# Kernel optimization log

Hardware: AMD Instinct MI355X
Metric: run time of the kernel (lower is better)

Reference implementation:

```python
import jax, jax.numpy as jnp
import numpy as np

B, Q, C, N_PER, GS = 8, 2048, 256, 64, 8
H1, H2 = 256, 64
EPS = 1e-5


def make_grid():
    a = jnp.linspace(-0.1, 0.1, GS)
    gx, gy = jnp.meshgrid(a, a, indexing='ij')  # torch.meshgrid default 'ij'
    return jnp.stack([gx.reshape(-1), gy.reshape(-1)], axis=1)  # (n, 2)


def setup_inputs() -> dict:
    key = jax.random.key(0)
    ks = jax.random.split(key, 10)
    s = lambda k, shp, fan: jax.random.normal(k, shp, jnp.float32) / np.sqrt(fan)
    return {
        'tokens': jax.random.normal(ks[0], (B, Q, C), jnp.float32),
        'grid': make_grid(),
        'Wc': s(ks[1], (C, 3), C), 'bc': jnp.zeros((3,), jnp.float32),
        'W1': s(ks[2], (C + 2, H1), C + 2), 'b1': jnp.zeros((H1,), jnp.float32),
        'gamma1': jnp.ones((H1,), jnp.float32), 'beta1': jnp.zeros((H1,), jnp.float32),
        'W2': s(ks[3], (H1, H2), H1), 'b2': jnp.zeros((H2,), jnp.float32),
        'gamma2': jnp.ones((H2,), jnp.float32), 'beta2': jnp.zeros((H2,), jnp.float32),
        'W3': s(ks[4], (H2, 3), H2), 'b3': jnp.zeros((3,), jnp.float32),
    }


def batchnorm(x, gamma, beta):
    # BatchNorm1d in training mode: stats over batch (B*Q) and length (n) dims,
    # per channel (last axis here).
    mean = jnp.mean(x, axis=(0, 1, 2), keepdims=True)
    var = jnp.var(x, axis=(0, 1, 2), keepdims=True)
    return gamma * (x - mean) * jax.lax.rsqrt(var + EPS) + beta


def reference(tokens, grid, Wc, bc, W1, b1, gamma1, beta1, W2, b2, gamma2, beta2, W3, b3):
    coarse = tokens @ Wc + bc  # (B, Q, 3)
    # conv1 (1x1) on concat([tokens_expanded, grid]) == split matmul + broadcast add;
    # avoids materializing the (B,Q,n,C+2) concat explicitly.
    tok_part = tokens @ W1[:C]                 # (B, Q, H1)
    grid_part = grid @ W1[C:]                  # (n, H1)
    h = tok_part[:, :, None, :] + grid_part[None, None, :, :] + b1  # (B, Q, n, H1)
    h = jax.nn.relu(batchnorm(h, gamma1, beta1))
    h = jnp.einsum('bqnc,cd->bqnd', h, W2) + b2  # (B, Q, n, H2)
    h = jax.nn.relu(batchnorm(h, gamma2, beta2))
    disp = jnp.einsum('bqnc,cd->bqnd', h, W3) + b3  # (B, Q, n, 3)
    fine = (coarse[:, :, None, :] + disp).reshape(B, Q * N_PER, 3)
    return coarse, fine
```

## Files before the change

kernel.cpp:

```cpp
#include <hip/hip_runtime.h>
#include <hip/hip_bf16.h>

#define ROWS 16384
#define C_   256
#define H1_  256
#define H2_  64
#define EPSN 1e-5f

typedef __bf16 bf16x8 __attribute__((ext_vector_type(8)));
typedef __bf16 bf16x4 __attribute__((ext_vector_type(4)));
typedef __bf16 bf16x2 __attribute__((ext_vector_type(2)));
typedef float  f32x4  __attribute__((ext_vector_type(4)));
typedef float  f32x2  __attribute__((ext_vector_type(2)));

__device__ __forceinline__ bf16x2 cvt2(float a, float b) {
#if __has_builtin(__builtin_amdgcn_cvt_pk_bf16_f32)
    return __builtin_bit_cast(bf16x2, __builtin_amdgcn_cvt_pk_bf16_f32(a, b));
#else
    bf16x2 r; r[0] = (__bf16)a; r[1] = (__bf16)b; return r;
#endif
}

__global__ __launch_bounds__(256) void k0_pack(const float* __restrict__ W1,
                                               const float* __restrict__ W2,
                                               const float* __restrict__ W3,
                                               __bf16* __restrict__ W1p,
                                               __bf16* __restrict__ W2p,
                                               __bf16* __restrict__ W3p,
                                               float* __restrict__ zero_base) {
    int idx = blockIdx.x * 256 + threadIdx.x;
    if (idx < 65536) {
        int j = idx & 7, l = (idx >> 3) & 63, rest = idx >> 9;
        int ks = rest & 7, CT = rest >> 3;
        int k = ks * 32 + ((l >> 4) << 3) + j;
        int c = CT * 16 + (l & 15);
        W1p[idx] = (__bf16)W1[k * H1_ + c];
    } else {
        int i2 = idx - 65536;
        int j = i2 & 7, l = (i2 >> 3) & 63, rest = i2 >> 9;
        int ks = rest & 7, CK = rest >> 3;
        int k = ks * 32 + ((l >> 4) << 3) + j;
        int c2 = CK * 16 + (l & 15);
        W2p[i2] = (__bf16)W2[k * H2_ + c2];
    }
    if (idx < 1024) {
        int j = idx & 7, l = (idx >> 3) & 63, ks = idx >> 9;
        int k = ks * 32 + ((l >> 4) << 3) + j;
        int c = l & 15;
        W3p[idx] = (c < 3) ? (__bf16)W3[k * 3 + c] : (__bf16)0.f;
    }
    if (idx < 24576) zero_base[idx] = 0.0f;
}

__device__ __forceinline__ void prep_ctx(const float* __restrict__ grid,
                                         const float* __restrict__ W1,
                                         const float* __restrict__ a1p, int c0,
                                         f32x2* wgx2, f32x2* wgy2, float* A_) {
#pragma unroll
    for (int j = 0; j < 8; ++j) A_[j] = grid[2 * j + 1];
    f32x4 a0 = *(const f32x4*)(a1p + c0), a1h = *(const f32x4*)(a1p + c0 + 4);
    f32x4 x0 = *(const f32x4*)(W1 + C_ * H1_ + c0), x1 = *(const f32x4*)(W1 + C_ * H1_ + c0 + 4);
    f32x4 y0 = *(const f32x4*)(W1 + (C_ + 1) * H1_ + c0), yh = *(const f32x4*)(W1 + (C_ + 1) * H1_ + c0 + 4);
    float av[8] = {a0[0], a0[1], a0[2], a0[3], a1h[0], a1h[1], a1h[2], a1h[3]};
    float wx[8] = {x0[0], x0[1], x0[2], x0[3], x1[0], x1[1], x1[2], x1[3]};
    float wy[8] = {y0[0], y0[1], y0[2], y0[3], yh[0], yh[1], yh[2], yh[3]};
#pragma unroll
    for (int e = 0; e < 4; ++e) {
        wgx2[e][0] = av[2 * e] * wx[2 * e];     wgx2[e][1] = av[2 * e + 1] * wx[2 * e + 1];
        wgy2[e][0] = av[2 * e] * wy[2 * e];     wgy2[e][1] = av[2 * e + 1] * wy[2 * e + 1];
    }
}

__device__ __forceinline__ void stage16(__bf16* __restrict__ y1, int w, int c0, int nh,
                                        const float* __restrict__ a1p,
                                        const float* __restrict__ d1p,
                                        const f32x2* wgx2, const f32x2* wgy2,
                                        const float* A_,
                                        const float* __restrict__ tokrow) {
    f32x4 t0 = *(const f32x4*)(tokrow + c0);
    f32x4 t1 = *(const f32x4*)(tokrow + c0 + 4);
    f32x4 a0 = *(const f32x4*)(a1p + c0), a1h = *(const f32x4*)(a1p + c0 + 4);
    f32x4 d0 = *(const f32x4*)(d1p + c0), d1h = *(const f32x4*)(d1p + c0 + 4);
    f32x2 base2[4];
    base2[0][0] = fmaf(a0[0], t0[0], d0[0]);  base2[0][1] = fmaf(a0[1], t0[1], d0[1]);
    base2[1][0] = fmaf(a0[2], t0[2], d0[2]);  base2[1][1] = fmaf(a0[3], t0[3], d0[3]);
    base2[2][0] = fmaf(a1h[0], t1[0], d1h[0]); base2[2][1] = fmaf(a1h[1], t1[1], d1h[1]);
    base2[3][0] = fmaf(a1h[2], t1[2], d1h[2]); base2[3][1] = fmaf(a1h[3], t1[3], d1h[3]);
#pragma unroll
    for (int ih = 0; ih < 2; ++ih) {
        float axs = A_[2 * w + ih];
        f32x2 ax2 = {axs, axs};
        f32x2 tc2[4];
#pragma unroll
        for (int e = 0; e < 4; ++e) tc2[e] = __builtin_elementwise_fma(wgx2[e], ax2, base2[e]);
#pragma unroll
        for (int kk = 0; kk < 4; ++kk) {
            int iy = nh + 2 * kk;
            float ays = A_[iy];
            f32x2 ay2 = {ays, ays};
            f32x2 z = {0.f, 0.f};
            int n = w * 16 + ih * 8 + iy;
            bf16x8 out;
            bf16x2* o2 = (bf16x2*)&out;
#pragma unroll
            for (int e = 0; e < 4; ++e) {
                f32x2 v = __builtin_elementwise_max(
                    __builtin_elementwise_fma(wgy2[e], ay2, tc2[e]), z);
                o2[e] = cvt2(v[0], v[1]);
            }
            *(bf16x8*)(&y1[n * 264 + c0]) = out;
        }
    }
}

__global__ __launch_bounds__(256) void k1a(const float* __restrict__ tokens,
                                           const __bf16* __restrict__ W1p,
                                           const float* __restrict__ Wc,
                                           const float* __restrict__ bc,
                                           float* __restrict__ tokpart,
                                           float* __restrict__ coarse,
                                           float* __restrict__ p1s,
                                           float* __restrict__ p1q) {
    __shared__ __align__(16) __bf16 Al[16 * 264];
    int t = threadIdx.x, w = t >> 6, l = t & 63;
    int quad = l >> 4, col = l & 15;
    int rowbase = (blockIdx.x >> 1) * 16;
    int colhalf = blockIdx.x & 1;
    int slot = blockIdx.x & 31;

    bf16x8 bfr[16];
#pragma unroll
    for (int ctl = 0; ctl < 2; ++ctl)
#pragma unroll
        for (int ks = 0; ks < 8; ++ks) {
            int CT = colhalf * 8 + w * 2 + ctl;
            bfr[ctl * 8 + ks] = *(const bf16x8*)(W1p + (((CT * 8 + ks) * 64 + l) * 8));
        }
    {
        int r = t >> 4, cb = (t & 15) * 16;
        const float* src = tokens + (size_t)(rowbase + r) * C_ + cb;
        f32x4 t0 = *(const f32x4*)(src);
        f32x4 t1 = *(const f32x4*)(src + 4);
        f32x4 t2 = *(const f32x4*)(src + 8);
        f32x4 t3 = *(const f32x4*)(src + 12);
        bf16x8 v0, v1;
        bf16x2* p0 = (bf16x2*)&v0; bf16x2* p1 = (bf16x2*)&v1;
        p0[0] = cvt2(t0[0], t0[1]); p0[1] = cvt2(t0[2], t0[3]);
        p0[2] = cvt2(t1[0], t1[1]); p0[3] = cvt2(t1[2], t1[3]);
        p1[0] = cvt2(t2[0], t2[1]); p1[1] = cvt2(t2[2], t2[3]);
        p1[2] = cvt2(t3[0], t3[1]); p1[3] = cvt2(t3[2], t3[3]);
        *(bf16x8*)(&Al[r * 264 + cb]) = v0;
        *(bf16x8*)(&Al[r * 264 + cb + 8]) = v1;
    }
    __syncthreads();

    bf16x8 af[8];
#pragma unroll
    for (int ks = 0; ks < 8; ++ks)
        af[ks] = *(const bf16x8*)(&Al[col * 264 + ks * 32 + quad * 8]);

#pragma unroll
    for (int ctl = 0; ctl < 2; ++ctl) {
        f32x4 acc = {0.f, 0.f, 0.f, 0.f};
#pragma unroll
        for (int ks = 0; ks < 8; ++ks)
            acc = __builtin_amdgcn_mfma_f32_16x16x32_bf16(af[ks], bfr[ctl * 8 + ks], acc, 0, 0, 0);
        int c = colhalf * 128 + w * 32 + ctl * 16 + col;
        float s = 0.f, q = 0.f;
#pragma unroll
        for (int rr = 0; rr < 4; ++rr) {
            float v = acc[rr];
            tokpart[(size_t)(rowbase + quad * 4 + rr) * C_ + c] = v;
            s += v; q += v * v;
        }
        s += __shfl_xor(s, 16, 64); s += __shfl_xor(s, 32, 64);
        q += __shfl_xor(q, 16, 64); q += __shfl_xor(q, 32, 64);
        if (l < 16) {
            int cc = colhalf * 128 + w * 32 + ctl * 16 + l;
            atomicAdd(p1s + slot * C_ + cc, s);
            atomicAdd(p1q + slot * C_ + cc, q);
        }
    }
    if (colhalf == 0) {
        const f32x4* wcp = (const f32x4*)(Wc + l * 12);
        f32x4 wa = wcp[0], wb = wcp[1], wv = wcp[2];
        float wcl[12] = {wa[0], wa[1], wa[2], wa[3], wb[0], wb[1], wb[2], wb[3],
                         wv[0], wv[1], wv[2], wv[3]};
#pragma unroll
        for (int rr = 0; rr < 4; ++rr) {
            int r = w * 4 + rr;
            bf16x4 tv4 = *(const bf16x4*)(&Al[r * 264 + l * 4]);
            float p[3] = {0.f, 0.f, 0.f};
#pragma unroll
            for (int i = 0; i < 4; ++i) {
                float tvf = (float)tv4[i];
#pragma unroll
                for (int j = 0; j < 3; ++j) p[j] = fmaf(tvf, wcl[i * 3 + j], p[j]);
            }
#pragma unroll
            for (int off = 1; off < 64; off <<= 1)
#pragma unroll
                for (int j = 0; j < 3; ++j) p[j] += __shfl_xor(p[j], off, 64);
            if (l == 0) {
#pragma unroll
                for (int j = 0; j < 3; ++j)
                    coarse[(size_t)(rowbase + r) * 3 + j] = p[j] + bc[j];
            }
        }
    }
}

__global__ void k1b(const float* __restrict__ grid, const float* __restrict__ W1,
                    const float* __restrict__ gamma1, const float* __restrict__ beta1,
                    const float* __restrict__ p1s, const float* __restrict__ p1q,
                    float* __restrict__ a1o, float* __restrict__ d1o) {
    int t = threadIdx.x;
    float S = 0.f, Qq = 0.f;
    for (int s = 0; s < 32; ++s) { S += p1s[s * C_ + t]; Qq += p1q[s * C_ + t]; }
    float mean_t = S / (float)ROWS;
    float var_t = Qq / (float)ROWS - mean_t * mean_t;
    float wx = W1[C_ * H1_ + t];
    float wy = W1[(C_ + 1) * H1_ + t];
    float mg = 0.f, qg = 0.f;
    for (int n = 0; n < 64; ++n) {
        float gv = grid[2 * n] * wx + grid[2 * n + 1] * wy;
        mg += gv; qg += gv * gv;
    }
    mg *= (1.f / 64.f);
    float var_g = qg * (1.f / 64.f) - mg * mg;
    float a1 = gamma1[t] * rsqrtf(var_t + var_g + EPSN);
    a1o[t] = a1;
    d1o[t] = beta1[t] - a1 * (mean_t + mg);
}

template <bool SPILL>
__global__ __launch_bounds__(256) void k2(const float* __restrict__ tokpart,
                                          const float* __restrict__ grid,
                                          const float* __restrict__ W1,
                                          const __bf16* __restrict__ W2p,
                                          const float* __restrict__ a1,
                                          const float* __restrict__ d1,
                                          float* __restrict__ p2s,
                                          float* __restrict__ p2q,
                                          __bf16* __restrict__ h2s) {
    __shared__ __align__(16) __bf16 y1[64 * 264];
    __shared__ __align__(16) __bf16 y2l[SPILL ? 64 * 72 : 8];
    int t = threadIdx.x, w = t >> 6, l = t & 63;
    int quad = l >> 4, col = l & 15;
    int wn = w >> 1, wc = w & 1;
    int c0 = (l & 31) * 8, nh = l >> 5;

    bf16x8 bfr[16];
#pragma unroll
    for (int ck = 0; ck < 2; ++ck)
#pragma unroll
        for (int ks = 0; ks < 8; ++ks)
            bfr[ck * 8 + ks] = *(const bf16x8*)(W2p + ((((wc * 2 + ck) * 8 + ks) * 64 + l) * 8));

    f32x2 wgx2[4], wgy2[4]; float A_[8];
    prep_ctx(grid, W1, a1, c0, wgx2, wgy2, A_);

    float s[2][4] = {}, q[2][4] = {};

#pragma unroll 1
    for (int r8 = 0; r8 < 8; ++r8) {
        int row = blockIdx.x * 8 + r8;
        stage16(y1, w, c0, nh, a1, d1, wgx2, wgy2, A_, tokpart + (size_t)row * C_);
        __syncthreads();
#pragma unroll
        for (int rt = 0; rt < 2; ++rt) {
            bf16x8 af[8];
#pragma unroll
            for (int ks = 0; ks < 8; ++ks)
                af[ks] = *(const bf16x8*)(&y1[(wn * 32 + rt * 16 + col) * 264 + ks * 32 + quad * 8]);
#pragma unroll
            for (int ck = 0; ck < 2; ++ck) {
                f32x4 acc = {0.f, 0.f, 0.f, 0.f};
#pragma unroll
                for (int ks = 0; ks < 8; ++ks)
                    acc = __builtin_amdgcn_mfma_f32_16x16x32_bf16(bfr[ck * 8 + ks], af[ks], acc, 0, 0, 0);
#pragma unroll
                for (int rr = 0; rr < 4; ++rr) {
                    s[ck][rr] += acc[rr];
                    q[ck][rr] += acc[rr] * acc[rr];
                }
                if constexpr (SPILL) {
                    bf16x4 v; bf16x2* v2 = (bf16x2*)&v;
                    v2[0] = cvt2(acc[0], acc[1]);
                    v2[1] = cvt2(acc[2], acc[3]);
                    *(bf16x4*)(&y2l[(wn * 32 + rt * 16 + col) * 72 + wc * 32 + ck * 16 + quad * 4]) = v;
                }
            }
        }
        __syncthreads();
        if constexpr (SPILL) {
            int n = t >> 2, cb = (t & 3) * 16;
            bf16x8 u0 = *(const bf16x8*)(&y2l[n * 72 + cb]);
            bf16x8 u1 = *(const bf16x8*)(&y2l[n * 72 + cb + 8]);
            __bf16* dst = h2s + (size_t)row * 4096 + t * 16;
            *(bf16x8*)dst = u0;
            *(bf16x8*)(dst + 8) = u1;
        }
    }
    int slot = blockIdx.x & 63;
#pragma unroll
    for (int ck = 0; ck < 2; ++ck)
#pragma unroll
        for (int rr = 0; rr < 4; ++rr) {
            float sv = s[ck][rr], qv = q[ck][rr];
            sv += __shfl_xor(sv, 1, 64); sv += __shfl_xor(sv, 2, 64);
            sv += __shfl_xor(sv, 4, 64); sv += __shfl_xor(sv, 8, 64);
            qv += __shfl_xor(qv, 1, 64); qv += __shfl_xor(qv, 2, 64);
            qv += __shfl_xor(qv, 4, 64); qv += __shfl_xor(qv, 8, 64);
            if (col == 0) {
                int c2 = wc * 32 + ck * 16 + quad * 4 + rr;
                atomicAdd(p2s + slot * H2_ + c2, sv);
                atomicAdd(p2q + slot * H2_ + c2, qv);
            }
        }
}

__global__ void k2b(const float* __restrict__ p2s, const float* __restrict__ p2q,
                    const float* __restrict__ gamma2, const float* __restrict__ beta2,
                    float* __restrict__ a2o, float* __restrict__ d2o) {
    int t = threadIdx.x;
    float S = 0.f, Qq = 0.f;
    for (int s = 0; s < 64; ++s) { S += p2s[s * H2_ + t]; Qq += p2q[s * H2_ + t]; }
    const float invN = 1.f / ((float)ROWS * 64.f);
    float mean = S * invN;
    float var = Qq * invN - mean * mean;
    float a2 = gamma2[t] * rsqrtf(var + EPSN);
    a2o[t] = a2;
    d2o[t] = beta2[t] - a2 * mean;
}

__global__ __launch_bounds__(256) void k3s(const __bf16* __restrict__ h2s,
                                           const float* __restrict__ a2,
                                           const float* __restrict__ d2p,
                                           const __bf16* __restrict__ W3p,
                                           const float* __restrict__ b3,
                                           const float* __restrict__ coarse,
                                           float* __restrict__ fine) {
    __shared__ __align__(16) __bf16 y2l[8][64 * 72];
    __shared__ __align__(16) float finebuf[8 * 192];
    int t = threadIdx.x, w = t >> 6, l = t & 63;
    int quad = l >> 4, col = l & 15;

    bf16x8 wfr[2];
#pragma unroll
    for (int ks = 0; ks < 2; ++ks)
        wfr[ks] = *(const bf16x8*)(W3p + ((ks * 64 + l) * 8));

    int n = t >> 2, cb = (t & 3) * 16;
    float a2r[16], d2r[16];
#pragma unroll
    for (int i = 0; i < 16; i += 4) {
        f32x4 av = *(const f32x4*)(a2 + cb + i);
        f32x4 dv = *(const f32x4*)(d2p + cb + i);
#pragma unroll
        for (int e = 0; e < 4; ++e) { a2r[i + e] = av[e]; d2r[i + e] = dv[e]; }
    }
#pragma unroll 1
    for (int r8 = 0; r8 < 8; ++r8) {
        size_t row = (size_t)blockIdx.x * 8 + r8;
        const __bf16* src = h2s + row * 4096 + t * 16;
        bf16x8 u0 = *(const bf16x8*)src;
        bf16x8 u1 = *(const bf16x8*)(src + 8);
        bf16x8 o0, o1;
        bf16x2* p0 = (bf16x2*)&o0; bf16x2* p1 = (bf16x2*)&o1;
#pragma unroll
        for (int e = 0; e < 4; ++e) {
            p0[e] = cvt2(fmaxf(fmaf(a2r[2 * e],     (float)u0[2 * e],     d2r[2 * e]), 0.f),
                         fmaxf(fmaf(a2r[2 * e + 1], (float)u0[2 * e + 1], d2r[2 * e + 1]), 0.f));
            p1[e] = cvt2(fmaxf(fmaf(a2r[8 + 2 * e],     (float)u1[2 * e],     d2r[8 + 2 * e]), 0.f),
                         fmaxf(fmaf(a2r[8 + 2 * e + 1], (float)u1[2 * e + 1], d2r[8 + 2 * e + 1]), 0.f));
        }
        *(bf16x8*)(&y2l[r8][n * 72 + cb]) = o0;
        *(bf16x8*)(&y2l[r8][n * 72 + cb + 8]) = o1;
    }
    __syncthreads();
    float b3v = (col < 3) ? b3[col] : 0.f;
#pragma unroll 1
    for (int r8 = 0; r8 < 8; ++r8) {
        int row = blockIdx.x * 8 + r8;
        bf16x8 af2[2];
#pragma unroll
        for (int ks = 0; ks < 2; ++ks)
            af2[ks] = *(const bf16x8*)(&y2l[r8][(w * 16 + col) * 72 + ks * 32 + quad * 8]);
        f32x4 acc = {0.f, 0.f, 0.f, 0.f};
        acc = __builtin_amdgcn_mfma_f32_16x16x32_bf16(af2[0], wfr[0], acc, 0, 0, 0);
        acc = __builtin_amdgcn_mfma_f32_16x16x32_bf16(af2[1], wfr[1], acc, 0, 0, 0);
        if (col < 3) {
            float cj = coarse[row * 3 + col] + b3v;
#pragma unroll
            for (int rr = 0; rr < 4; ++rr)
                finebuf[r8 * 192 + (w * 16 + quad * 4 + rr) * 3 + col] = acc[rr] + cj;
        }
    }
    __syncthreads();
    {
        float* dst = fine + (size_t)blockIdx.x * 1536;
        const f32x4* fb = (const f32x4*)finebuf;
        *(f32x4*)(dst + 4 * t) = fb[t];
        if (t < 128) *(f32x4*)(dst + 1024 + 4 * t) = fb[256 + t];
    }
}

__global__ __launch_bounds__(256) void k3r(const float* __restrict__ tokpart,
                                           const float* __restrict__ grid,
                                           const float* __restrict__ W1,
                                           const __bf16* __restrict__ W2p,
                                           const float* __restrict__ a1,
                                           const float* __restrict__ d1,
                                           const __bf16* __restrict__ W3p,
                                           const float* __restrict__ a2,
                                           const float* __restrict__ d2p,
                                           const float* __restrict__ b3,
                                           const float* __restrict__ coarse,
                                           float* __restrict__ fine) {
    __shared__ __align__(16) __bf16 y1[64 * 264];
    __shared__ __align__(16) __bf16 y2l[64 * 72];
    __shared__ __align__(16) float finebuf[8 * 192];
    int t = threadIdx.x, w = t >> 6, l = t & 63;
    int quad = l >> 4, col = l & 15;
    int wn = w >> 1, wc = w & 1;
    int c0 = (l & 31) * 8, nh = l >> 5;

    bf16x8 bfr[16];
#pragma unroll
    for (int ck = 0; ck < 2; ++ck)
#pragma unroll
        for (int ks = 0; ks < 8; ++ks)
            bfr[ck * 8 + ks] = *(const bf16x8*)(W2p + ((((wc * 2 + ck) * 8 + ks) * 64 + l) * 8));
    bf16x8 wfr[2];
#pragma unroll
    for (int ks = 0; ks < 2; ++ks)
        wfr[ks] = *(const bf16x8*)(W3p + ((ks * 64 + l) * 8));

    f32x2 wgx2[4], wgy2[4]; float A_[8];
    prep_ctx(grid, W1, a1, c0, wgx2, wgy2, A_);

    float a2v[8], d2v[8];
#pragma unroll
    for (int ck = 0; ck < 2; ++ck)
#pragma unroll
        for (int rr = 0; rr < 4; ++rr) {
            int c2 = wc * 32 + ck * 16 + quad * 4 + rr;
            a2v[ck * 4 + rr] = a2[c2];
            d2v[ck * 4 + rr] = d2p[c2];
        }
    float b3v = (col < 3) ? b3[col] : 0.f;

#pragma unroll 1
    for (int r8 = 0; r8 < 8; ++r8) {
        int row = blockIdx.x * 8 + r8;
        stage16(y1, w, c0, nh, a1, d1, wgx2, wgy2, A_, tokpart + (size_t)row * C_);
        __syncthreads();
#pragma unroll
        for (int rt = 0; rt < 2; ++rt) {
            bf16x8 af[8];
#pragma unroll
            for (int ks = 0; ks < 8; ++ks)
                af[ks] = *(const bf16x8*)(&y1[(wn * 32 + rt * 16 + col) * 264 + ks * 32 + quad * 8]);
#pragma unroll
            for (int ck = 0; ck < 2; ++ck) {
                f32x4 acc = {0.f, 0.f, 0.f, 0.f};
#pragma unroll
                for (int ks = 0; ks < 8; ++ks)
                    acc = __builtin_amdgcn_mfma_f32_16x16x32_bf16(bfr[ck * 8 + ks], af[ks], acc, 0, 0, 0);
                bf16x4 v; bf16x2* v2 = (bf16x2*)&v;
                float y0 = fmaxf(fmaf(a2v[ck * 4 + 0], acc[0], d2v[ck * 4 + 0]), 0.f);
                float y1v = fmaxf(fmaf(a2v[ck * 4 + 1], acc[1], d2v[ck * 4 + 1]), 0.f);
                float y2 = fmaxf(fmaf(a2v[ck * 4 + 2], acc[2], d2v[ck * 4 + 2]), 0.f);
                float y3 = fmaxf(fmaf(a2v[ck * 4 + 3], acc[3], d2v[ck * 4 + 3]), 0.f);
                v2[0] = cvt2(y0, y1v); v2[1] = cvt2(y2, y3);
                *(bf16x4*)(&y2l[(wn * 32 + rt * 16 + col) * 72 + wc * 32 + ck * 16 + quad * 4]) = v;
            }
        }
        __syncthreads();
        bf16x8 af2[2];
#pragma unroll
        for (int ks = 0; ks < 2; ++ks)
            af2[ks] = *(const bf16x8*)(&y2l[(w * 16 + col) * 72 + ks * 32 + quad * 8]);
        f32x4 d2acc = {0.f, 0.f, 0.f, 0.f};
        d2acc = __builtin_amdgcn_mfma_f32_16x16x32_bf16(af2[0], wfr[0], d2acc, 0, 0, 0);
        d2acc = __builtin_amdgcn_mfma_f32_16x16x32_bf16(af2[1], wfr[1], d2acc, 0, 0, 0);
        if (col < 3) {
            float cj = coarse[row * 3 + col] + b3v;
#pragma unroll
            for (int rr = 0; rr < 4; ++rr)
                finebuf[r8 * 192 + (w * 16 + quad * 4 + rr) * 3 + col] = d2acc[rr] + cj;
        }
    }
    __syncthreads();
    {
        float* dst = fine + (size_t)blockIdx.x * 1536;
        const f32x4* fb = (const f32x4*)finebuf;
        *(f32x4*)(dst + 4 * t) = fb[t];
        if (t < 128) *(f32x4*)(dst + 1024 + 4 * t) = fb[256 + t];
    }
}

extern "C" void kernel_launch(void* const* d_in, const int* in_sizes, int n_in,
                              void* d_out, int out_size, void* d_ws, size_t ws_size,
                              hipStream_t stream) {
    (void)in_sizes; (void)n_in; (void)out_size;
    const float* tokens = (const float*)d_in[0];
    const float* grid   = (const float*)d_in[1];
    const float* Wc     = (const float*)d_in[2];
    const float* bc     = (const float*)d_in[3];
    const float* W1     = (const float*)d_in[4];
    const float* gamma1 = (const float*)d_in[6];
    const float* beta1  = (const float*)d_in[7];
    const float* W2     = (const float*)d_in[8];
    const float* gamma2 = (const float*)d_in[10];
    const float* beta2  = (const float*)d_in[11];
    const float* W3     = (const float*)d_in[12];
    const float* b3     = (const float*)d_in[13];

    char* ws = (char*)d_ws;
    __bf16* W1p     = (__bf16*)(ws);
    __bf16* W2p     = (__bf16*)(ws + 131072);
    float*  p1s     = (float*)(ws + 163840);
    float*  p1q     = (float*)(ws + 196608);
    float*  p2s     = (float*)(ws + 229376);
    float*  p2q     = (float*)(ws + 245760);
    float*  a1      = (float*)(ws + 262144);
    float*  d1      = (float*)(ws + 263168);
    float*  a2      = (float*)(ws + 264192);
    float*  d2p     = (float*)(ws + 264448);
    __bf16* W3p     = (__bf16*)(ws + 264704);
    float*  tokpart = (float*)(ws + 266752);
    __bf16* h2s     = (__bf16*)(ws + 17043968);

    const size_t SPILL_NEED = 17043968ull + 134217728ull;
    bool spill = ws_size >= SPILL_NEED;

    float* coarse = (float*)d_out;
    float* fine   = (float*)d_out + (size_t)ROWS * 3;

    k0_pack<<<320, 256, 0, stream>>>(W1, W2, W3, W1p, W2p, W3p, p1s);
    k1a<<<2048, 256, 0, stream>>>(tokens, W1p, Wc, bc, tokpart, coarse, p1s, p1q);
    k1b<<<1, 256, 0, stream>>>(grid, W1, gamma1, beta1, p1s, p1q, a1, d1);
    if (spill) {
        k2<true><<<ROWS / 8, 256, 0, stream>>>(tokpart, grid, W1, W2p, a1, d1, p2s, p2q, h2s);
        k2b<<<1, 64, 0, stream>>>(p2s, p2q, gamma2, beta2, a2, d2p);
        k3s<<<ROWS / 8, 256, 0, stream>>>(h2s, a2, d2p, W3p, b3, coarse, fine);
    } else {
        k2<false><<<ROWS / 8, 256, 0, stream>>>(tokpart, grid, W1, W2p, a1, d1, p2s, p2q, h2s);
        k2b<<<1, 64, 0, stream>>>(p2s, p2q, gamma2, beta2, a2, d2p);
        k3r<<<ROWS / 8, 256, 0, stream>>>(tokpart, grid, W1, W2p, a1, d1, W3p, a2, d2p, b3, coarse, fine);
    }
}
```

Measured before the change: 212.4 us.

## Build layer-1 activations in registers and recompute layer 2 instead of spilling

The BN1 affine is pre-folded into the token projection (kfold), and the grid contribution is precomputed per lane. Each lane then forms its MFMA A-fragment directly in registers, so the y1 shared-memory staging and its barriers go away. The h2 spill path is dropped, and layer 2 is recomputed in k3x. Blocks now cover half of the 64 grid points, which doubles the grid size. This trades the 128MB bf16 spill round trip, plus LDS traffic, for one extra fp32 tokfold buffer and repeated per-lane token loads.

```diff
diff --git a/kernel.cpp b/kernel.cpp
--- a/kernel.cpp
+++ b/kernel.cpp
@@ -52,67 +52,6 @@
     if (idx < 24576) zero_base[idx] = 0.0f;
 }
 
-__device__ __forceinline__ void prep_ctx(const float* __restrict__ grid,
-                                         const float* __restrict__ W1,
-                                         const float* __restrict__ a1p, int c0,
-                                         f32x2* wgx2, f32x2* wgy2, float* A_) {
-#pragma unroll
-    for (int j = 0; j < 8; ++j) A_[j] = grid[2 * j + 1];
-    f32x4 a0 = *(const f32x4*)(a1p + c0), a1h = *(const f32x4*)(a1p + c0 + 4);
-    f32x4 x0 = *(const f32x4*)(W1 + C_ * H1_ + c0), x1 = *(const f32x4*)(W1 + C_ * H1_ + c0 + 4);
-    f32x4 y0 = *(const f32x4*)(W1 + (C_ + 1) * H1_ + c0), yh = *(const f32x4*)(W1 + (C_ + 1) * H1_ + c0 + 4);
-    float av[8] = {a0[0], a0[1], a0[2], a0[3], a1h[0], a1h[1], a1h[2], a1h[3]};
-    float wx[8] = {x0[0], x0[1], x0[2], x0[3], x1[0], x1[1], x1[2], x1[3]};
-    float wy[8] = {y0[0], y0[1], y0[2], y0[3], yh[0], yh[1], yh[2], yh[3]};
-#pragma unroll
-    for (int e = 0; e < 4; ++e) {
-        wgx2[e][0] = av[2 * e] * wx[2 * e];     wgx2[e][1] = av[2 * e + 1] * wx[2 * e + 1];
-        wgy2[e][0] = av[2 * e] * wy[2 * e];     wgy2[e][1] = av[2 * e + 1] * wy[2 * e + 1];
-    }
-}
-
-__device__ __forceinline__ void stage16(__bf16* __restrict__ y1, int w, int c0, int nh,
-                                        const float* __restrict__ a1p,
-                                        const float* __restrict__ d1p,
-                                        const f32x2* wgx2, const f32x2* wgy2,
-                                        const float* A_,
-                                        const float* __restrict__ tokrow) {
-    f32x4 t0 = *(const f32x4*)(tokrow + c0);
-    f32x4 t1 = *(const f32x4*)(tokrow + c0 + 4);
-    f32x4 a0 = *(const f32x4*)(a1p + c0), a1h = *(const f32x4*)(a1p + c0 + 4);
-    f32x4 d0 = *(const f32x4*)(d1p + c0), d1h = *(const f32x4*)(d1p + c0 + 4);
-    f32x2 base2[4];
-    base2[0][0] = fmaf(a0[0], t0[0], d0[0]);  base2[0][1] = fmaf(a0[1], t0[1], d0[1]);
-    base2[1][0] = fmaf(a0[2], t0[2], d0[2]);  base2[1][1] = fmaf(a0[3], t0[3], d0[3]);
-    base2[2][0] = fmaf(a1h[0], t1[0], d1h[0]); base2[2][1] = fmaf(a1h[1], t1[1], d1h[1]);
-    base2[3][0] = fmaf(a1h[2], t1[2], d1h[2]); base2[3][1] = fmaf(a1h[3], t1[3], d1h[3]);
-#pragma unroll
-    for (int ih = 0; ih < 2; ++ih) {
-        float axs = A_[2 * w + ih];
-        f32x2 ax2 = {axs, axs};
-        f32x2 tc2[4];
-#pragma unroll
-        for (int e = 0; e < 4; ++e) tc2[e] = __builtin_elementwise_fma(wgx2[e], ax2, base2[e]);
-#pragma unroll
-        for (int kk = 0; kk < 4; ++kk) {
-            int iy = nh + 2 * kk;
-            float ays = A_[iy];
-            f32x2 ay2 = {ays, ays};
-            f32x2 z = {0.f, 0.f};
-            int n = w * 16 + ih * 8 + iy;
-            bf16x8 out;
-            bf16x2* o2 = (bf16x2*)&out;
-#pragma unroll
-            for (int e = 0; e < 4; ++e) {
-                f32x2 v = __builtin_elementwise_max(
-                    __builtin_elementwise_fma(wgy2[e], ay2, tc2[e]), z);
-                o2[e] = cvt2(v[0], v[1]);
-            }
-            *(bf16x8*)(&y1[n * 264 + c0]) = out;
-        }
-    }
-}
-
 __global__ __launch_bounds__(256) void k1a(const float* __restrict__ tokens,
                                            const __bf16* __restrict__ W1p,
                                            const float* __restrict__ Wc,
@@ -213,7 +152,8 @@
 __global__ void k1b(const float* __restrict__ grid, const float* __restrict__ W1,
                     const float* __restrict__ gamma1, const float* __restrict__ beta1,
                     const float* __restrict__ p1s, const float* __restrict__ p1q,
-                    float* __restrict__ a1o, float* __restrict__ d1o) {
+                    float* __restrict__ a1o, float* __restrict__ d1o,
+                    float* __restrict__ wgxo, float* __restrict__ wgyo) {
     int t = threadIdx.x;
     float S = 0.f, Qq = 0.f;
     for (int s = 0; s < 32; ++s) { S += p1s[s * C_ + t]; Qq += p1q[s * C_ + t]; }
@@ -231,93 +171,101 @@
     float a1 = gamma1[t] * rsqrtf(var_t + var_g + EPSN);
     a1o[t] = a1;
     d1o[t] = beta1[t] - a1 * (mean_t + mg);
-}
-
-template <bool SPILL>
-__global__ __launch_bounds__(256) void k2(const float* __restrict__ tokpart,
-                                          const float* __restrict__ grid,
-                                          const float* __restrict__ W1,
-                                          const __bf16* __restrict__ W2p,
-                                          const float* __restrict__ a1,
-                                          const float* __restrict__ d1,
-                                          float* __restrict__ p2s,
-                                          float* __restrict__ p2q,
-                                          __bf16* __restrict__ h2s) {
-    __shared__ __align__(16) __bf16 y1[64 * 264];
-    __shared__ __align__(16) __bf16 y2l[SPILL ? 64 * 72 : 8];
+    wgxo[t] = a1 * wx;
+    wgyo[t] = a1 * wy;
+}
+
+__global__ __launch_bounds__(256) void kfold(const float* __restrict__ tokpart,
+                                             const float* __restrict__ a1,
+                                             const float* __restrict__ d1,
+                                             float* __restrict__ tokfold) {
+    int idx = blockIdx.x * 256 + threadIdx.x;
+    int c0 = (idx * 4) & 255;
+    f32x4 a = *(const f32x4*)(a1 + c0);
+    f32x4 d = *(const f32x4*)(d1 + c0);
+    f32x4 v = *(const f32x4*)(tokpart + (size_t)idx * 4);
+    *(f32x4*)(tokfold + (size_t)idx * 4) = __builtin_elementwise_fma(a, v, d);
+}
+
+__global__ __launch_bounds__(256) void k2x(const float* __restrict__ tokfold,
+                                           const float* __restrict__ grid,
+                                           const __bf16* __restrict__ W2p,
+                                           const float* __restrict__ wgx,
+                                           const float* __restrict__ wgy,
+                                           float* __restrict__ p2s,
+                                           float* __restrict__ p2q) {
     int t = threadIdx.x, w = t >> 6, l = t & 63;
     int quad = l >> 4, col = l & 15;
     int wn = w >> 1, wc = w & 1;
-    int c0 = (l & 31) * 8, nh = l >> 5;
+    int rowgrp = blockIdx.x >> 1, nh = blockIdx.x & 1;
+    int n = nh * 32 + wn * 16 + col;
+    float gx = grid[2 * n], gy = grid[2 * n + 1];
 
     bf16x8 bfr[16];
 #pragma unroll
     for (int ck = 0; ck < 2; ++ck)
 #pragma unroll
-        for (int ks = 0; ks < 8; ++ks)
-            bfr[ck * 8 + ks] = *(const bf16x8*)(W2p + ((((wc * 2 + ck) * 8 + ks) * 64 + l) * 8));
-
-    f32x2 wgx2[4], wgy2[4]; float A_[8];
-    prep_ctx(grid, W1, a1, c0, wgx2, wgy2, A_);
-
-    float s[2][4] = {}, q[2][4] = {};
+        for (int ks = 0; ks < 8; ++ks) {
+            int CK = wc * 2 + ck;
+            bfr[ck * 8 + ks] = *(const bf16x8*)(W2p + (((CK * 8 + ks) * 64 + l) * 8));
+        }
+
+    f32x4 gt[16];
+    f32x4 gx4 = {gx, gx, gx, gx}, gy4 = {gy, gy, gy, gy};
+#pragma unroll
+    for (int ks = 0; ks < 8; ++ks) {
+        int cb = ks * 32 + quad * 8;
+        f32x4 wx0 = *(const f32x4*)(wgx + cb), wx1 = *(const f32x4*)(wgx + cb + 4);
+        f32x4 wy0 = *(const f32x4*)(wgy + cb), wy1 = *(const f32x4*)(wgy + cb + 4);
+        gt[2 * ks]     = __builtin_elementwise_fma(gy4, wy0, gx4 * wx0);
+        gt[2 * ks + 1] = __builtin_elementwise_fma(gy4, wy1, gx4 * wx1);
+    }
+
+    float s[8] = {}, q[8] = {};
+    const f32x4 z4 = {0.f, 0.f, 0.f, 0.f};
 
 #pragma unroll 1
     for (int r8 = 0; r8 < 8; ++r8) {
-        int row = blockIdx.x * 8 + r8;
-        stage16(y1, w, c0, nh, a1, d1, wgx2, wgy2, A_, tokpart + (size_t)row * C_);
-        __syncthreads();
-#pragma unroll
-        for (int rt = 0; rt < 2; ++rt) {
-            bf16x8 af[8];
+        const float* tr = tokfold + (size_t)(rowgrp * 8 + r8) * C_;
+        bf16x8 af[8];
+#pragma unroll
+        for (int ks = 0; ks < 8; ++ks) {
+            int cb = ks * 32 + quad * 8;
+            f32x4 t0 = *(const f32x4*)(tr + cb);
+            f32x4 t1 = *(const f32x4*)(tr + cb + 4);
+            f32x4 v0 = __builtin_elementwise_max(t0 + gt[2 * ks], z4);
+            f32x4 v1 = __builtin_elementwise_max(t1 + gt[2 * ks + 1], z4);
+            bf16x2* o = (bf16x2*)&af[ks];
+            o[0] = cvt2(v0[0], v0[1]); o[1] = cvt2(v0[2], v0[3]);
+            o[2] = cvt2(v1[0], v1[1]); o[3] = cvt2(v1[2], v1[3]);
+        }
+#pragma unroll
+        for (int ck = 0; ck < 2; ++ck) {
+            f32x4 acc = {0.f, 0.f, 0.f, 0.f};
 #pragma unroll
             for (int ks = 0; ks < 8; ++ks)
-                af[ks] = *(const bf16x8*)(&y1[(wn * 32 + rt * 16 + col) * 264 + ks * 32 + quad * 8]);
-#pragma unroll
-            for (int ck = 0; ck < 2; ++ck) {
-                f32x4 acc = {0.f, 0.f, 0.f, 0.f};
-#pragma unroll
-                for (int ks = 0; ks < 8; ++ks)
-                    acc = __builtin_amdgcn_mfma_f32_16x16x32_bf16(bfr[ck * 8 + ks], af[ks], acc, 0, 0, 0);
-#pragma unroll
-                for (int rr = 0; rr < 4; ++rr) {
-                    s[ck][rr] += acc[rr];
-                    q[ck][rr] += acc[rr] * acc[rr];
-                }
-                if constexpr (SPILL) {
-                    bf16x4 v; bf16x2* v2 = (bf16x2*)&v;
-                    v2[0] = cvt2(acc[0], acc[1]);
-                    v2[1] = cvt2(acc[2], acc[3]);
-                    *(bf16x4*)(&y2l[(wn * 32 + rt * 16 + col) * 72 + wc * 32 + ck * 16 + quad * 4]) = v;
-                }
+                acc = __builtin_amdgcn_mfma_f32_16x16x32_bf16(bfr[ck * 8 + ks], af[ks], acc, 0, 0, 0);
+#pragma unroll
+            for (int rr = 0; rr < 4; ++rr) {
+                s[ck * 4 + rr] += acc[rr];
+                q[ck * 4 + rr] = fmaf(acc[rr], acc[rr], q[ck * 4 + rr]);
             }
         }
-        __syncthreads();
-        if constexpr (SPILL) {
-            int n = t >> 2, cb = (t & 3) * 16;
-            bf16x8 u0 = *(const bf16x8*)(&y2l[n * 72 + cb]);
-            bf16x8 u1 = *(const bf16x8*)(&y2l[n * 72 + cb + 8]);
-            __bf16* dst = h2s + (size_t)row * 4096 + t * 16;
-            *(bf16x8*)dst = u0;
-            *(bf16x8*)(dst + 8) = u1;
-        }
     }
     int slot = blockIdx.x & 63;
 #pragma unroll
-    for (int ck = 0; ck < 2; ++ck)
-#pragma unroll
-        for (int rr = 0; rr < 4; ++rr) {
-            float sv = s[ck][rr], qv = q[ck][rr];
-            sv += __shfl_xor(sv, 1, 64); sv += __shfl_xor(sv, 2, 64);
-            sv += __shfl_xor(sv, 4, 64); sv += __shfl_xor(sv, 8, 64);
-            qv += __shfl_xor(qv, 1, 64); qv += __shfl_xor(qv, 2, 64);
-            qv += __shfl_xor(qv, 4, 64); qv += __shfl_xor(qv, 8, 64);
-            if (col == 0) {
-                int c2 = wc * 32 + ck * 16 + quad * 4 + rr;
-                atomicAdd(p2s + slot * H2_ + c2, sv);
-                atomicAdd(p2q + slot * H2_ + c2, qv);
-            }
-        }
+    for (int i = 0; i < 8; ++i) {
+        float sv = s[i], qv = q[i];
+        sv += __shfl_xor(sv, 1, 64); sv += __shfl_xor(sv, 2, 64);
+        sv += __shfl_xor(sv, 4, 64); sv += __shfl_xor(sv, 8, 64);
+        qv += __shfl_xor(qv, 1, 64); qv += __shfl_xor(qv, 2, 64);
+        qv += __shfl_xor(qv, 4, 64); qv += __shfl_xor(qv, 8, 64);
+        if (col == 0) {
+            int c2 = wc * 32 + (i >> 2) * 16 + quad * 4 + (i & 3);
+            atomicAdd(p2s + slot * H2_ + c2, sv);
+            atomicAdd(p2q + slot * H2_ + c2, qv);
+        }
+    }
 }
 
 __global__ void k2b(const float* __restrict__ p2s, const float* __restrict__ p2q,
@@ -334,177 +282,122 @@
     d2o[t] = beta2[t] - a2 * mean;
 }
 
-__global__ __launch_bounds__(256) void k3s(const __bf16* __restrict__ h2s,
+__global__ __launch_bounds__(256) void k3x(const float* __restrict__ tokfold,
+                                           const float* __restrict__ grid,
+                                           const __bf16* __restrict__ W2p,
+                                           const float* __restrict__ wgx,
+                                           const float* __restrict__ wgy,
                                            const float* __restrict__ a2,
                                            const float* __restrict__ d2p,
                                            const __bf16* __restrict__ W3p,
                                            const float* __restrict__ b3,
                                            const float* __restrict__ coarse,
                                            float* __restrict__ fine) {
-    __shared__ __align__(16) __bf16 y2l[8][64 * 72];
-    __shared__ __align__(16) float finebuf[8 * 192];
+    __shared__ __align__(16) __bf16 y2l[8 * 32 * 72];
+    __shared__ __align__(16) float finebuf[8 * 96];
     int t = threadIdx.x, w = t >> 6, l = t & 63;
     int quad = l >> 4, col = l & 15;
-
+    int wn = w >> 1, wc = w & 1;
+    int rowgrp = blockIdx.x >> 1, nh = blockIdx.x & 1;
+    int n = nh * 32 + wn * 16 + col;
+    float gx = grid[2 * n], gy = grid[2 * n + 1];
+
+    bf16x8 bfr[16];
+#pragma unroll
+    for (int ck = 0; ck < 2; ++ck)
+#pragma unroll
+        for (int ks = 0; ks < 8; ++ks) {
+            int CK = wc * 2 + ck;
+            bfr[ck * 8 + ks] = *(const bf16x8*)(W2p + (((CK * 8 + ks) * 64 + l) * 8));
+        }
+    f32x4 gt[16];
+    f32x4 gx4 = {gx, gx, gx, gx}, gy4 = {gy, gy, gy, gy};
+#pragma unroll
+    for (int ks = 0; ks < 8; ++ks) {
+        int cb = ks * 32 + quad * 8;
+        f32x4 wx0 = *(const f32x4*)(wgx + cb), wx1 = *(const f32x4*)(wgx + cb + 4);
+        f32x4 wy0 = *(const f32x4*)(wgy + cb), wy1 = *(const f32x4*)(wgy + cb + 4);
+        gt[2 * ks]     = __builtin_elementwise_fma(gy4, wy0, gx4 * wx0);
+        gt[2 * ks + 1] = __builtin_elementwise_fma(gy4, wy1, gx4 * wx1);
+    }
+    float a2v[8], d2v[8];
+#pragma unroll
+    for (int ck = 0; ck < 2; ++ck)
+#pragma unroll
+        for (int rr = 0; rr < 4; ++rr) {
+            int c2 = wc * 32 + ck * 16 + quad * 4 + rr;
+            a2v[ck * 4 + rr] = a2[c2];
+            d2v[ck * 4 + rr] = d2p[c2];
+        }
+    const f32x4 z4 = {0.f, 0.f, 0.f, 0.f};
+
+#pragma unroll 1
+    for (int r8 = 0; r8 < 8; ++r8) {
+        const float* tr = tokfold + (size_t)(rowgrp * 8 + r8) * C_;
+        bf16x8 af[8];
+#pragma unroll
+        for (int ks = 0; ks < 8; ++ks) {
+            int cb = ks * 32 + quad * 8;
+            f32x4 t0 = *(const f32x4*)(tr + cb);
+            f32x4 t1 = *(const f32x4*)(tr + cb + 4);
+            f32x4 v0 = __builtin_elementwise_max(t0 + gt[2 * ks], z4);
+            f32x4 v1 = __builtin_elementwise_max(t1 + gt[2 * ks + 1], z4);
+            bf16x2* o = (bf16x2*)&af[ks];
+            o[0] = cvt2(v0[0], v0[1]); o[1] = cvt2(v0[2], v0[3]);
+            o[2] = cvt2(v1[0], v1[1]); o[3] = cvt2(v1[2], v1[3]);
+        }
+#pragma unroll
+        for (int ck = 0; ck < 2; ++ck) {
+            f32x4 acc = {0.f, 0.f, 0.f, 0.f};
+#pragma unroll
+            for (int ks = 0; ks < 8; ++ks)
+                acc = __builtin_amdgcn_mfma_f32_16x16x32_bf16(bfr[ck * 8 + ks], af[ks], acc, 0, 0, 0);
+            bf16x4 v; bf16x2* v2 = (bf16x2*)&v;
+            float y0 = fmaxf(fmaf(a2v[ck * 4 + 0], acc[0], d2v[ck * 4 + 0]), 0.f);
+            float y1 = fmaxf(fmaf(a2v[ck * 4 + 1], acc[1], d2v[ck * 4 + 1]), 0.f);
+            float y2 = fmaxf(fmaf(a2v[ck * 4 + 2], acc[2], d2v[ck * 4 + 2]), 0.f);
+            float y3 = fmaxf(fmaf(a2v[ck * 4 + 3], acc[3], d2v[ck * 4 + 3]), 0.f);
+            v2[0] = cvt2(y0, y1); v2[1] = cvt2(y2, y3);
+            *(bf16x4*)(&y2l[r8 * 2304 + (wn * 16 + col) * 72 + wc * 32 + ck * 16 + quad * 4]) = v;
+        }
+    }
+    __syncthreads();
     bf16x8 wfr[2];
 #pragma unroll
     for (int ks = 0; ks < 2; ++ks)
         wfr[ks] = *(const bf16x8*)(W3p + ((ks * 64 + l) * 8));
-
-    int n = t >> 2, cb = (t & 3) * 16;
-    float a2r[16], d2r[16];
-#pragma unroll
-    for (int i = 0; i < 16; i += 4) {
-        f32x4 av = *(const f32x4*)(a2 + cb + i);
-        f32x4 dv = *(const f32x4*)(d2p + cb + i);
-#pragma unroll
-        for (int e = 0; e < 4; ++e) { a2r[i + e] = av[e]; d2r[i + e] = dv[e]; }
-    }
-#pragma unroll 1
-    for (int r8 = 0; r8 < 8; ++r8) {
-        size_t row = (size_t)blockIdx.x * 8 + r8;
-        const __bf16* src = h2s + row * 4096 + t * 16;
-        bf16x8 u0 = *(const bf16x8*)src;
-        bf16x8 u1 = *(const bf16x8*)(src + 8);
-        bf16x8 o0, o1;
-        bf16x2* p0 = (bf16x2*)&o0; bf16x2* p1 = (bf16x2*)&o1;
-#pragma unroll
-        for (int e = 0; e < 4; ++e) {
-            p0[e] = cvt2(fmaxf(fmaf(a2r[2 * e],     (float)u0[2 * e],     d2r[2 * e]), 0.f),
-                         fmaxf(fmaf(a2r[2 * e + 1], (float)u0[2 * e + 1], d2r[2 * e + 1]), 0.f));
-            p1[e] = cvt2(fmaxf(fmaf(a2r[8 + 2 * e],     (float)u1[2 * e],     d2r[8 + 2 * e]), 0.f),
-                         fmaxf(fmaf(a2r[8 + 2 * e + 1], (float)u1[2 * e + 1], d2r[8 + 2 * e + 1]), 0.f));
-        }
-        *(bf16x8*)(&y2l[r8][n * 72 + cb]) = o0;
-        *(bf16x8*)(&y2l[r8][n * 72 + cb + 8]) = o1;
-    }
-    __syncthreads();
     float b3v = (col < 3) ? b3[col] : 0.f;
-#pragma unroll 1
-    for (int r8 = 0; r8 < 8; ++r8) {
-        int row = blockIdx.x * 8 + r8;
+#pragma unroll
+    for (int i = 0; i < 4; ++i) {
+        int tt = w * 4 + i;
+        int r8 = tt >> 1, nt = tt & 1;
         bf16x8 af2[2];
 #pragma unroll
-        for (int ks = 0; ks < 2; ++ks)
-            af2[ks] = *(const bf16x8*)(&y2l[r8][(w * 16 + col) * 72 + ks * 32 + quad * 8]);
+        for (int k2 = 0; k2 < 2; ++k2)
+            af2[k2] = *(const bf16x8*)(&y2l[r8 * 2304 + (nt * 16 + col) * 72 + k2 * 32 + quad * 8]);
         f32x4 acc = {0.f, 0.f, 0.f, 0.f};
         acc = __builtin_amdgcn_mfma_f32_16x16x32_bf16(af2[0], wfr[0], acc, 0, 0, 0);
         acc = __builtin_amdgcn_mfma_f32_16x16x32_bf16(af2[1], wfr[1], acc, 0, 0, 0);
         if (col < 3) {
+            int row = rowgrp * 8 + r8;
             float cj = coarse[row * 3 + col] + b3v;
 #pragma unroll
             for (int rr = 0; rr < 4; ++rr)
-                finebuf[r8 * 192 + (w * 16 + quad * 4 + rr) * 3 + col] = acc[rr] + cj;
+                finebuf[r8 * 96 + (nt * 16 + quad * 4 + rr) * 3 + col] = acc[rr] + cj;
         }
     }
     __syncthreads();
-    {
-        float* dst = fine + (size_t)blockIdx.x * 1536;
-        const f32x4* fb = (const f32x4*)finebuf;
-        *(f32x4*)(dst + 4 * t) = fb[t];
-        if (t < 128) *(f32x4*)(dst + 1024 + 4 * t) = fb[256 + t];
-    }
-}
-
-__global__ __launch_bounds__(256) void k3r(const float* __restrict__ tokpart,
-                                           const float* __restrict__ grid,
-                                           const float* __restrict__ W1,
-                                           const __bf16* __restrict__ W2p,
-                                           const float* __restrict__ a1,
-                                           const float* __restrict__ d1,
-                                           const __bf16* __restrict__ W3p,
-                                           const float* __restrict__ a2,
-                                           const float* __restrict__ d2p,
-                                           const float* __restrict__ b3,
-                                           const float* __restrict__ coarse,
-                                           float* __restrict__ fine) {
-    __shared__ __align__(16) __bf16 y1[64 * 264];
-    __shared__ __align__(16) __bf16 y2l[64 * 72];
-    __shared__ __align__(16) float finebuf[8 * 192];
-    int t = threadIdx.x, w = t >> 6, l = t & 63;
-    int quad = l >> 4, col = l & 15;
-    int wn = w >> 1, wc = w & 1;
-    int c0 = (l & 31) * 8, nh = l >> 5;
-
-    bf16x8 bfr[16];
-#pragma unroll
-    for (int ck = 0; ck < 2; ++ck)
-#pragma unroll
-        for (int ks = 0; ks < 8; ++ks)
-            bfr[ck * 8 + ks] = *(const bf16x8*)(W2p + ((((wc * 2 + ck) * 8 + ks) * 64 + l) * 8));
-    bf16x8 wfr[2];
-#pragma unroll
-    for (int ks = 0; ks < 2; ++ks)
-        wfr[ks] = *(const bf16x8*)(W3p + ((ks * 64 + l) * 8));
-
-    f32x2 wgx2[4], wgy2[4]; float A_[8];
-    prep_ctx(grid, W1, a1, c0, wgx2, wgy2, A_);
-
-    float a2v[8], d2v[8];
-#pragma unroll
-    for (int ck = 0; ck < 2; ++ck)
-#pragma unroll
-        for (int rr = 0; rr < 4; ++rr) {
-            int c2 = wc * 32 + ck * 16 + quad * 4 + rr;
-            a2v[ck * 4 + rr] = a2[c2];
-            d2v[ck * 4 + rr] = d2p[c2];
-        }
-    float b3v = (col < 3) ? b3[col] : 0.f;
-
-#pragma unroll 1
-    for (int r8 = 0; r8 < 8; ++r8) {
-        int row = blockIdx.x * 8 + r8;
-        stage16(y1, w, c0, nh, a1, d1, wgx2, wgy2, A_, tokpart + (size_t)row * C_);
-        __syncthreads();
-#pragma unroll
-        for (int rt = 0; rt < 2; ++rt) {
-            bf16x8 af[8];
-#pragma unroll
-            for (int ks = 0; ks < 8; ++ks)
-                af[ks] = *(const bf16x8*)(&y1[(wn * 32 + rt * 16 + col) * 264 + ks * 32 + quad * 8]);
-#pragma unroll
-            for (int ck = 0; ck < 2; ++ck) {
-                f32x4 acc = {0.f, 0.f, 0.f, 0.f};
-#pragma unroll
-                for (int ks = 0; ks < 8; ++ks)
-                    acc = __builtin_amdgcn_mfma_f32_16x16x32_bf16(bfr[ck * 8 + ks], af[ks], acc, 0, 0, 0);
-                bf16x4 v; bf16x2* v2 = (bf16x2*)&v;
-                float y0 = fmaxf(fmaf(a2v[ck * 4 + 0], acc[0], d2v[ck * 4 + 0]), 0.f);
-                float y1v = fmaxf(fmaf(a2v[ck * 4 + 1], acc[1], d2v[ck * 4 + 1]), 0.f);
-                float y2 = fmaxf(fmaf(a2v[ck * 4 + 2], acc[2], d2v[ck * 4 + 2]), 0.f);
-                float y3 = fmaxf(fmaf(a2v[ck * 4 + 3], acc[3], d2v[ck * 4 + 3]), 0.f);
-                v2[0] = cvt2(y0, y1v); v2[1] = cvt2(y2, y3);
-                *(bf16x4*)(&y2l[(wn * 32 + rt * 16 + col) * 72 + wc * 32 + ck * 16 + quad * 4]) = v;
-            }
-        }
-        __syncthreads();
-        bf16x8 af2[2];
-#pragma unroll
-        for (int ks = 0; ks < 2; ++ks)
-            af2[ks] = *(const bf16x8*)(&y2l[(w * 16 + col) * 72 + ks * 32 + quad * 8]);
-        f32x4 d2acc = {0.f, 0.f, 0.f, 0.f};
-        d2acc = __builtin_amdgcn_mfma_f32_16x16x32_bf16(af2[0], wfr[0], d2acc, 0, 0, 0);
-        d2acc = __builtin_amdgcn_mfma_f32_16x16x32_bf16(af2[1], wfr[1], d2acc, 0, 0, 0);
-        if (col < 3) {
-            float cj = coarse[row * 3 + col] + b3v;
-#pragma unroll
-            for (int rr = 0; rr < 4; ++rr)
-                finebuf[r8 * 192 + (w * 16 + quad * 4 + rr) * 3 + col] = d2acc[rr] + cj;
-        }
-    }
-    __syncthreads();
-    {
-        float* dst = fine + (size_t)blockIdx.x * 1536;
-        const f32x4* fb = (const f32x4*)finebuf;
-        *(f32x4*)(dst + 4 * t) = fb[t];
-        if (t < 128) *(f32x4*)(dst + 1024 + 4 * t) = fb[256 + t];
+    if (t < 192) {
+        int r8 = t / 24, wi = t - r8 * 24;
+        float* dst = fine + ((size_t)(rowgrp * 8 + r8) * 64 + nh * 32) * 3 + wi * 4;
+        *(f32x4*)dst = ((const f32x4*)finebuf)[t];
     }
 }
 
 extern "C" void kernel_launch(void* const* d_in, const int* in_sizes, int n_in,
                               void* d_out, int out_size, void* d_ws, size_t ws_size,
                               hipStream_t stream) {
-    (void)in_sizes; (void)n_in; (void)out_size;
+    (void)in_sizes; (void)n_in; (void)out_size; (void)ws_size;
     const float* tokens = (const float*)d_in[0];
     const float* grid   = (const float*)d_in[1];
     const float* Wc     = (const float*)d_in[2];
@@ -530,25 +423,19 @@
     float*  a2      = (float*)(ws + 264192);
     float*  d2p     = (float*)(ws + 264448);
     __bf16* W3p     = (__bf16*)(ws + 264704);
-    float*  tokpart = (float*)(ws + 266752);
-    __bf16* h2s     = (__bf16*)(ws + 17043968);
-
-    const size_t SPILL_NEED = 17043968ull + 134217728ull;
-    bool spill = ws_size >= SPILL_NEED;
+    float*  wgx     = (float*)(ws + 266752);
+    float*  wgy     = (float*)(ws + 267776);
+    float*  tokpart = (float*)(ws + 268800);
+    float*  tokfold = (float*)(ws + 17046016);
 
     float* coarse = (float*)d_out;
     float* fine   = (float*)d_out + (size_t)ROWS * 3;
 
     k0_pack<<<320, 256, 0, stream>>>(W1, W2, W3, W1p, W2p, W3p, p1s);
     k1a<<<2048, 256, 0, stream>>>(tokens, W1p, Wc, bc, tokpart, coarse, p1s, p1q);
-    k1b<<<1, 256, 0, stream>>>(grid, W1, gamma1, beta1, p1s, p1q, a1, d1);
-    if (spill) {
-        k2<true><<<ROWS / 8, 256, 0, stream>>>(tokpart, grid, W1, W2p, a1, d1, p2s, p2q, h2s);
-        k2b<<<1, 64, 0, stream>>>(p2s, p2q, gamma2, beta2, a2, d2p);
-        k3s<<<ROWS / 8, 256, 0, stream>>>(h2s, a2, d2p, W3p, b3, coarse, fine);
-    } else {
-        k2<false><<<ROWS / 8, 256, 0, stream>>>(tokpart, grid, W1, W2p, a1, d1, p2s, p2q, h2s);
-        k2b<<<1, 64, 0, stream>>>(p2s, p2q, gamma2, beta2, a2, d2p);
-        k3r<<<ROWS / 8, 256, 0, stream>>>(tokpart, grid, W1, W2p, a1, d1, W3p, a2, d2p, b3, coarse, fine);
-    }
-}
+    k1b<<<1, 256, 0, stream>>>(grid, W1, gamma1, beta1, p1s, p1q, a1, d1, wgx, wgy);
+    kfold<<<4096, 256, 0, stream>>>(tokpart, a1, d1, tokfold);
+    k2x<<<4096, 256, 0, stream>>>(tokfold, grid, W2p, wgx, wgy, p2s, p2q);
+    k2b<<<1, 64, 0, stream>>>(p2s, p2q, gamma2, beta2, a2, d2p);
+    k3x<<<4096, 256, 0, stream>>>(tokfold, grid, W2p, wgx, wgy, a2, d2p, W3p, b3, coarse, fine);
+}
```

Result: slower. 314.3 us (+48.0%).
